# Kernel tuning notes

Hardware: AMD Instinct MI355X
Metric: run time of the kernel (lower is better)

Reference implementation:

```python
import jax, jax.numpy as jnp
import numpy as np

H = 512
V = 32000
B = 32
S = 64
T = 32  # max_len


def setup_inputs() -> dict:
    key = jax.random.key(0)
    ks = jax.random.split(key, 16)
    sc = 0.02
    return {
        'encoder_outputs': jax.random.normal(ks[0], (B, S, 2 * H), jnp.float32),
        'encoder_hidden': jax.random.normal(ks[1], (1, B, 2 * H), jnp.float32),
        'target_tensor': jax.random.randint(ks[2], (B, T), 0, V),
        'emb': sc * jax.random.normal(ks[3], (V, H), jnp.float32),
        'Wa_w': sc * jax.random.normal(ks[4], (H, H), jnp.float32),
        'Wa_b': jnp.zeros((H,), jnp.float32),
        'Ua_w': sc * jax.random.normal(ks[5], (H, 2 * H), jnp.float32),
        'Ua_b': jnp.zeros((H,), jnp.float32),
        'Va_w': sc * jax.random.normal(ks[6], (1, H), jnp.float32),
        'Va_b': jnp.zeros((1,), jnp.float32),
        'W_ih': sc * jax.random.normal(ks[7], (3 * H, 3 * H), jnp.float32),
        'b_ih': jnp.zeros((3 * H,), jnp.float32),
        'W_hh': sc * jax.random.normal(ks[8], (3 * H, H), jnp.float32),
        'b_hh': jnp.zeros((3 * H,), jnp.float32),
        'Wh': sc * jax.random.normal(ks[9], (H, 2 * H), jnp.float32),
        'bh': jnp.zeros((H,), jnp.float32),
        'out_w': sc * jax.random.normal(ks[10], (V, H), jnp.float32),
        'out_b': jnp.zeros((V,), jnp.float32),
    }


def reference(encoder_outputs, encoder_hidden, target_tensor, emb,
              Wa_w, Wa_b, Ua_w, Ua_b, Va_w, Va_b,
              W_ih, b_ih, W_hh, b_hh, Wh, bh, out_w, out_b):
    # initial hidden: Linear(2H -> H) applied to encoder_hidden [1,B,2H]
    h0 = encoder_hidden[0] @ Wh.T + bh  # [B,H]
    # Ua(keys) is step-invariant: precompute  [B,S,H]
    ua_keys = jnp.einsum('bsk,hk->bsh', encoder_outputs, Ua_w) + Ua_b
    # teacher forcing: first token is 0 (SOS), then shifted targets
    tokens = jnp.concatenate(
        [jnp.zeros((target_tensor.shape[0], 1), target_tensor.dtype),
         target_tensor[:, :-1]], axis=1)  # [B,T]

    def step(h, tok):
        x_emb = emb[tok]  # [B,H] (dropout is identity in eval)
        q = h @ Wa_w.T + Wa_b  # [B,H]
        e = jnp.tanh(q[:, None, :] + ua_keys)  # [B,S,H]
        scores = jnp.einsum('bsh,h->bs', e, Va_w[0]) + Va_b[0]  # [B,S]
        w = jax.nn.softmax(scores, axis=-1)  # [B,S]
        ctx = jnp.einsum('bs,bsk->bk', w, encoder_outputs)  # [B,2H]
        x = jnp.concatenate([x_emb, ctx], axis=-1)  # [B,3H]
        gx = x @ W_ih.T + b_ih  # [B,3H]
        gh = h @ W_hh.T + b_hh  # [B,3H]
        r = jax.nn.sigmoid(gx[:, :H] + gh[:, :H])
        z = jax.nn.sigmoid(gx[:, H:2 * H] + gh[:, H:2 * H])
        n = jnp.tanh(gx[:, 2 * H:] + r * gh[:, 2 * H:])
        h_new = (1.0 - z) * n + z * h
        logits = h_new @ out_w.T + out_b  # [B,V]
        return h_new, (logits, w)

    h_final, (logits, attn) = jax.lax.scan(step, h0, tokens.T)
    logits = jnp.transpose(logits, (1, 0, 2))  # [B,T,V]
    attn = jnp.transpose(attn, (1, 0, 2))  # [B,T,S]
    log_probs = jax.nn.log_softmax(logits, axis=-1)
    return log_probs, h_final[None], attn
```

## Files before the change

### kernel.cpp

```cpp
#include <hip/hip_runtime.h>
#include <hip/hip_bf16.h>

#define B_ 32
#define S_ 64
#define H_ 512
#define T_ 32
#define V_ 32000

typedef __attribute__((ext_vector_type(8))) short bf16x8;
typedef __attribute__((ext_vector_type(4))) float f32x4;

static __device__ __forceinline__ unsigned short f2bf(float f) {
    unsigned int u = __float_as_uint(f);
    u += 0x7FFF + ((u >> 16) & 1);
    return (unsigned short)(u >> 16);
}
static __device__ __forceinline__ float dot4(float4 a, float4 b) {
    return a.x * b.x + a.y * b.y + a.z * b.z + a.w * b.w;
}
static __device__ __forceinline__ float tanh_fast(float x) {
    x = fminf(fmaxf(x, -15.f), 15.f);
    float e = __expf(2.f * x);
    return (e - 1.f) / (e + 1.f);
}
static __device__ __forceinline__ float sigmoid_fast(float x) {
    return 1.f / (1.f + __expf(-x));
}

static __device__ __forceinline__ void gemm_tile_f32(
    const float* __restrict__ A, int Ald,
    const float* __restrict__ Bm, int Bld,
    const float* __restrict__ bias,
    float* __restrict__ C, int Cld,
    int m0, int n0, int k0beg, int k0end)
{
    __shared__ unsigned short As[128 * 32];
    __shared__ unsigned short Bs[128 * 32];

    const int tid  = threadIdx.x;
    const int lane = tid & 63;
    const int wave = tid >> 6;
    const int wm   = (wave & 1) * 64;
    const int wn   = (wave >> 1) * 64;
    const int quad = lane >> 4;
    const int l16  = lane & 15;

    f32x4 acc[4][4];
#pragma unroll
    for (int i = 0; i < 4; i++)
#pragma unroll
        for (int j = 0; j < 4; j++) acc[i][j] = (f32x4){0.f, 0.f, 0.f, 0.f};

    const int r0 = tid >> 2;
    const int q4 = tid & 3;

    for (int k0 = k0beg; k0 < k0end; k0 += 32) {
        __syncthreads();
#pragma unroll
        for (int rr = 0; rr < 2; rr++) {
            const int row = r0 + rr * 64;
            const float4 s0 = *(const float4*)(A + (size_t)(m0 + row) * Ald + k0 + q4 * 8);
            const float4 s1 = *(const float4*)(A + (size_t)(m0 + row) * Ald + k0 + q4 * 8 + 4);
            unsigned short tmp[8] = {f2bf(s0.x), f2bf(s0.y), f2bf(s0.z), f2bf(s0.w),
                                     f2bf(s1.x), f2bf(s1.y), f2bf(s1.z), f2bf(s1.w)};
            *(uint4*)(&As[row * 32 + q4 * 8]) = *(uint4*)tmp;
            const float4 t0 = *(const float4*)(Bm + (size_t)(n0 + row) * Bld + k0 + q4 * 8);
            const float4 t1 = *(const float4*)(Bm + (size_t)(n0 + row) * Bld + k0 + q4 * 8 + 4);
            unsigned short tb[8] = {f2bf(t0.x), f2bf(t0.y), f2bf(t0.z), f2bf(t0.w),
                                    f2bf(t1.x), f2bf(t1.y), f2bf(t1.z), f2bf(t1.w)};
            *(uint4*)(&Bs[row * 32 + q4 * 8]) = *(uint4*)tb;
        }
        __syncthreads();

        bf16x8 af[4], bfr[4];
#pragma unroll
        for (int i = 0; i < 4; i++)
            af[i] = *(const bf16x8*)(&As[(wm + 16 * i + l16) * 32 + quad * 8]);
#pragma unroll
        for (int j = 0; j < 4; j++)
            bfr[j] = *(const bf16x8*)(&Bs[(wn + 16 * j + l16) * 32 + quad * 8]);
#pragma unroll
        for (int i = 0; i < 4; i++)
#pragma unroll
            for (int j = 0; j < 4; j++)
                acc[i][j] = __builtin_amdgcn_mfma_f32_16x16x32_bf16(af[i], bfr[j], acc[i][j], 0, 0, 0);
    }

#pragma unroll
    for (int i = 0; i < 4; i++)
#pragma unroll
        for (int j = 0; j < 4; j++)
#pragma unroll
            for (int r = 0; r < 4; r++) {
                const int m = m0 + wm + 16 * i + quad * 4 + r;
                const int n = n0 + wn + 16 * j + l16;
                C[(size_t)m * Cld + n] = acc[i][j][r] + (bias ? bias[n] : 0.f);
            }
}

__global__ __launch_bounds__(256, 2)
void gemm_setup(const float* __restrict__ enc, const float* __restrict__ Xemb,
                const float* __restrict__ Ua_w, const float* __restrict__ W_ih,
                const float* __restrict__ b_ih,
                float* __restrict__ Pua, float* __restrict__ Gxe,
                float* __restrict__ Penc2)
{
    const int bid = blockIdx.x;
    if (bid < 128) {
        const int kk = bid & 1, l = bid >> 1;
        const int mt = l & 15, nt = l >> 4;
        gemm_tile_f32(enc, 1024, Ua_w, 1024, nullptr,
                      Pua + (size_t)kk * 1048576, 512,
                      mt * 128, nt * 128, kk * 512, kk * 512 + 512);
    } else if (bid < 224) {
        const int l = bid - 128;
        const int mt = l & 7, nt = l >> 3;
        gemm_tile_f32(Xemb, 512, W_ih, 1536, b_ih,
                      Gxe, 1536, mt * 128, nt * 128, 0, 512);
    } else {
        int l = bid - 224;
        const int kk = l & 1; l >>= 1;
        const int mt = l & 15, nt = l >> 4;
        gemm_tile_f32(enc, 1024, W_ih + 512, 1536, nullptr,
                      Penc2 + (size_t)kk * 3145728, 1536,
                      mt * 128, nt * 128, kk * 512, kk * 512 + 512);
    }
}

__global__ void k_combine(const float* __restrict__ Pua, const float* __restrict__ Ua_b,
                          float* __restrict__ ua, const float* __restrict__ Penc2,
                          float* __restrict__ ENC2)
{
    const int o = blockIdx.x * 256 + threadIdx.x;
    if (o < 262144) {
        const float4 a = ((const float4*)Pua)[o];
        const float4 b = ((const float4*)Pua)[262144 + o];
        const float4 bi = *(const float4*)(Ua_b + (o & 127) * 4);
        float4 r; r.x = a.x + b.x + bi.x; r.y = a.y + b.y + bi.y;
        r.z = a.z + b.z + bi.z; r.w = a.w + b.w + bi.w;
        ((float4*)ua)[o] = r;
    } else {
        const int i = o - 262144;
        const float4 a = ((const float4*)Penc2)[i];
        const float4 b = ((const float4*)Penc2)[786432 + i];
        float4 r; r.x = a.x + b.x; r.y = a.y + b.y; r.z = a.z + b.z; r.w = a.w + b.w;
        ((float4*)ENC2)[i] = r;
    }
}

__global__ __launch_bounds__(256, 2)
void gemm_logits(const unsigned short* __restrict__ A16, const float* __restrict__ Bm,
                 const float* __restrict__ bias, float* __restrict__ C)
{
    const int bid = blockIdx.x;
    const int xcd = bid & 7;
    const int l   = bid >> 3;
    const int nt  = (l >> 3) * 8 + xcd;
    if (nt >= 250) return;
    const int m0 = (l & 7) * 128;
    const int n0 = nt * 128;
    const int N = V_, K = 512, Bld = 512;

    __shared__ unsigned short As[128 * 32];
    __shared__ unsigned short Bs[128 * 32];

    const int tid  = threadIdx.x;
    const int lane = tid & 63;
    const int wave = tid >> 6;
    const int wm   = (wave & 1) * 64;
    const int wn   = (wave >> 1) * 64;
    const int quad = lane >> 4;
    const int l16  = lane & 15;

    f32x4 acc[4][4];
#pragma unroll
    for (int i = 0; i < 4; i++)
#pragma unroll
        for (int j = 0; j < 4; j++) acc[i][j] = (f32x4){0.f, 0.f, 0.f, 0.f};

    const int r0 = tid >> 2;
    const int q4 = tid & 3;

    for (int k0 = 0; k0 < K; k0 += 32) {
        __syncthreads();
#pragma unroll
        for (int rr = 0; rr < 2; rr++) {
            const int row = r0 + rr * 64;
            const uint4 v = *(const uint4*)(A16 + (size_t)(m0 + row) * K + k0 + q4 * 8);
            *(uint4*)(&As[row * 32 + q4 * 8]) = v;
            const float4 t0 = *(const float4*)(Bm + (size_t)(n0 + row) * Bld + k0 + q4 * 8);
            const float4 t1 = *(const float4*)(Bm + (size_t)(n0 + row) * Bld + k0 + q4 * 8 + 4);
            unsigned short tb[8] = {f2bf(t0.x), f2bf(t0.y), f2bf(t0.z), f2bf(t0.w),
                                    f2bf(t1.x), f2bf(t1.y), f2bf(t1.z), f2bf(t1.w)};
            *(uint4*)(&Bs[row * 32 + q4 * 8]) = *(uint4*)tb;
        }
        __syncthreads();

        bf16x8 af[4], bfr[4];
#pragma unroll
        for (int i = 0; i < 4; i++)
            af[i] = *(const bf16x8*)(&As[(wm + 16 * i + l16) * 32 + quad * 8]);
#pragma unroll
        for (int j = 0; j < 4; j++)
            bfr[j] = *(const bf16x8*)(&Bs[(wn + 16 * j + l16) * 32 + quad * 8]);
#pragma unroll
        for (int i = 0; i < 4; i++)
#pragma unroll
            for (int j = 0; j < 4; j++)
                acc[i][j] = __builtin_amdgcn_mfma_f32_16x16x32_bf16(af[i], bfr[j], acc[i][j], 0, 0, 0);
    }

#pragma unroll
    for (int i = 0; i < 4; i++)
#pragma unroll
        for (int j = 0; j < 4; j++)
#pragma unroll
            for (int r = 0; r < 4; r++) {
                const int m = m0 + wm + 16 * i + quad * 4 + r;
                const int n = n0 + wn + 16 * j + l16;
                C[(size_t)m * N + n] = acc[i][j][r] + bias[n];
            }
}

__global__ void k_h0part(const float* __restrict__ ehid, const float* __restrict__ Wh,
                         float* __restrict__ h0p)
{
    const int o = blockIdx.x * 256 + threadIdx.x;
    const int b = o & 31, j = (o >> 5) & 511, c = o >> 14;
    const float* x = ehid + b * 1024 + c * 256;
    const float* w = Wh + (size_t)j * 1024 + c * 256;
    float s = 0.f;
#pragma unroll 8
    for (int k = 0; k < 256; k += 4)
        s += dot4(*(const float4*)(x + k), *(const float4*)(w + k));
    h0p[c * 16384 + b * 512 + j] = s;
}

__global__ void k_h0fin(const float* __restrict__ h0p, const float* __restrict__ bh,
                        float* __restrict__ h)
{
    const int o = blockIdx.x * 256 + threadIdx.x;
    h[o] = bh[o & 511] + h0p[o] + h0p[16384 + o] + h0p[32768 + o] + h0p[49152 + o];
}

__global__ void k_gather(const float* __restrict__ emb, const int* __restrict__ tgt,
                         float* __restrict__ Xemb)
{
    const int o = blockIdx.x * 256 + threadIdx.x;
    const int r = o >> 7, k4 = (o & 127) * 4;
    const int b = r >> 5, t = r & 31;
    const int tok = t ? tgt[b * T_ + t - 1] : 0;
    *(float4*)(Xemb + (size_t)r * 512 + k4) = *(const float4*)(emb + (size_t)tok * 512 + k4);
}

__global__ __launch_bounds__(256)
void k_q_gh(const float* __restrict__ h, const float* __restrict__ Wa_w,
            const float* __restrict__ W_hh,
            float* __restrict__ qp, float* __restrict__ ghp)
{
    const int bid = blockIdx.x;
    const int tid = threadIdx.x;
    if (bid < 256) {
        const int o = bid * 256 + tid;
        const int b = o & 31, j = (o >> 5) & 511, c = o >> 14;
        const float* x = h + b * 512 + c * 128;
        const float* w = Wa_w + (size_t)j * 512 + c * 128;
        float s = 0.f;
#pragma unroll 8
        for (int k = 0; k < 128; k += 4)
            s += dot4(*(const float4*)(x + k), *(const float4*)(w + k));
        qp[c * 16384 + b * 512 + j] = s;
    } else {
        const int o = (bid - 256) * 256 + tid;
        const int b = o & 31, j = (o >> 5) & 511, c = o >> 14;
        const float* x  = h + b * 512 + c * 128;
        const float* w0 = W_hh + (size_t)j * 512 + c * 128;
        const float* w1 = w0 + 512 * 512;
        const float* w2 = w1 + 512 * 512;
        float s0 = 0.f, s1 = 0.f, s2 = 0.f;
#pragma unroll 8
        for (int k = 0; k < 128; k += 4) {
            const float4 xv = *(const float4*)(x + k);
            s0 += dot4(xv, *(const float4*)(w0 + k));
            s1 += dot4(xv, *(const float4*)(w1 + k));
            s2 += dot4(xv, *(const float4*)(w2 + k));
        }
        const int ix = b * 512 + j;
        ghp[(c * 3 + 0) * 16384 + ix] = s0;
        ghp[(c * 3 + 1) * 16384 + ix] = s1;
        ghp[(c * 3 + 2) * 16384 + ix] = s2;
    }
}

__global__ __launch_bounds__(256)
void k_attn_fin(const float* __restrict__ qp, const float* __restrict__ Wa_b,
                const float* __restrict__ ua, const float* __restrict__ Va_w,
                const float* __restrict__ Va_b, const float* __restrict__ ENC2,
                const float* __restrict__ ghp, const float* __restrict__ Gxe,
                const float* __restrict__ b_hh, float* __restrict__ h,
                unsigned short* __restrict__ Hall, float* __restrict__ attn_out,
                float* __restrict__ hf, int t)
{
    __shared__ float qs[512];
    __shared__ float parts[64][4];
    __shared__ float wsm[64];
    __shared__ float gxs[1536];

    const int b = blockIdx.x;
    const int tid = threadIdx.x;

    for (int i = tid; i < 512; i += 256) {
        const int ix = b * 512 + i;
        qs[i] = qp[ix] + qp[16384 + ix] + qp[32768 + ix] + qp[49152 + ix] + Wa_b[i];
    }
    __syncthreads();

    {
        const int s = tid >> 2, p = tid & 3;
        const float* uar = ua + ((size_t)(b * 64 + s)) * 512 + p * 128;
        const float* vp = Va_w + p * 128;
        float acc = 0.f;
#pragma unroll 8
        for (int k = 0; k < 128; k += 4) {
            float4 u4 = *(const float4*)(uar + k);
            float4 v4 = *(const float4*)(vp + k);
            float4 q4 = *(const float4*)(&qs[p * 128 + k]);
            acc += v4.x * tanh_fast(q4.x + u4.x) + v4.y * tanh_fast(q4.y + u4.y)
                 + v4.z * tanh_fast(q4.z + u4.z) + v4.w * tanh_fast(q4.w + u4.w);
        }
        parts[s][p] = acc;
    }
    __syncthreads();

    if (tid < 64) {
        float sc = parts[tid][0] + parts[tid][1] + parts[tid][2] + parts[tid][3] + Va_b[0];
        float mx = sc;
        for (int off = 32; off; off >>= 1) mx = fmaxf(mx, __shfl_down(mx, off));
        mx = __shfl(mx, 0);
        float e = __expf(sc - mx);
        float sum = e;
        for (int off = 32; off; off >>= 1) sum += __shfl_down(sum, off);
        sum = __shfl(sum, 0);
        float w = e / sum;
        wsm[tid] = w;
        attn_out[((size_t)b * T_ + t) * 64 + tid] = w;
    }
    __syncthreads();

    for (int i4 = tid; i4 < 384; i4 += 256) {
        float4 a = {0.f, 0.f, 0.f, 0.f};
        const float* eb = ENC2 + ((size_t)b * 64) * 1536 + i4 * 4;
        for (int s2 = 0; s2 < 64; s2++) {
            const float w = wsm[s2];
            const float4 e4 = *(const float4*)(eb + (size_t)s2 * 1536);
            a.x += w * e4.x; a.y += w * e4.y; a.z += w * e4.z; a.w += w * e4.w;
        }
        *(float4*)(&gxs[i4 * 4]) = a;
    }
    __syncthreads();

    for (int j = tid; j < 512; j += 256) {
        const int o2 = b * 512 + j;
        float gh0 = b_hh[j], gh1 = b_hh[512 + j], gh2 = b_hh[1024 + j];
#pragma unroll
        for (int c2 = 0; c2 < 4; c2++) {
            gh0 += ghp[(c2 * 3 + 0) * 16384 + o2];
            gh1 += ghp[(c2 * 3 + 1) * 16384 + o2];
            gh2 += ghp[(c2 * 3 + 2) * 16384 + o2];
        }
        const float* gxe = Gxe + ((size_t)(b * T_ + t)) * 1536;
        const float gx0 = gxs[j] + gxe[j];
        const float gx1 = gxs[512 + j] + gxe[512 + j];
        const float gx2 = gxs[1024 + j] + gxe[1024 + j];
        const float r = sigmoid_fast(gx0 + gh0);
        const float z = sigmoid_fast(gx1 + gh1);
        const float n = tanh_fast(gx2 + r * gh2);
        const float hn = (1.f - z) * n + z * h[o2];
        h[o2] = hn;
        Hall[((size_t)b * T_ + t) * 512 + j] = f2bf(hn);
        if (t == T_ - 1) hf[o2] = hn;
    }
}

__global__ void k_logsoftmax(float* __restrict__ logits)
{
    __shared__ float rm[4], rs[4];
    const int row = blockIdx.x;
    float* p = logits + (size_t)row * V_;
    const int tid = threadIdx.x;

    float m = -1e30f, s = 0.f;
    for (int i = tid * 4; i < V_; i += 1024) {
        const float4 x = *(const float4*)(p + i);
        const float m4 = fmaxf(fmaxf(x.x, x.y), fmaxf(x.z, x.w));
        const float mn = fmaxf(m, m4);
        s = s * __expf(m - mn) + __expf(x.x - mn) + __expf(x.y - mn)
          + __expf(x.z - mn) + __expf(x.w - mn);
        m = mn;
    }
    for (int off = 32; off; off >>= 1) {
        const float m2 = __shfl_down(m, off), s2 = __shfl_down(s, off);
        const float mn = fmaxf(m, m2);
        s = s * __expf(m - mn) + s2 * __expf(m2 - mn);
        m = mn;
    }
    if ((tid & 63) == 0) { rm[tid >> 6] = m; rs[tid >> 6] = s; }
    __syncthreads();
    const float M = fmaxf(fmaxf(rm[0], rm[1]), fmaxf(rm[2], rm[3]));
    const float S = rs[0] * __expf(rm[0] - M) + rs[1] * __expf(rm[1] - M)
                  + rs[2] * __expf(rm[2] - M) + rs[3] * __expf(rm[3] - M);
    const float lse = M + __logf(S);

    for (int i = tid * 4; i < V_; i += 1024) {
        float4 x = *(const float4*)(p + i);
        x.x -= lse; x.y -= lse; x.z -= lse; x.w -= lse;
        *(float4*)(p + i) = x;
    }
}

extern "C" void kernel_launch(void* const* d_in, const int* in_sizes, int n_in,
                              void* d_out, int out_size, void* d_ws, size_t ws_size,
                              hipStream_t stream)
{
    const float* enc   = (const float*)d_in[0];
    const float* ehid  = (const float*)d_in[1];
    const int*   tgt   = (const int*)d_in[2];
    const float* emb   = (const float*)d_in[3];
    const float* Wa_w  = (const float*)d_in[4];
    const float* Wa_b  = (const float*)d_in[5];
    const float* Ua_w  = (const float*)d_in[6];
    const float* Ua_b  = (const float*)d_in[7];
    const float* Va_w  = (const float*)d_in[8];
    const float* Va_b  = (const float*)d_in[9];
    const float* W_ih  = (const float*)d_in[10];
    const float* b_ih  = (const float*)d_in[11];
    const float* W_hh  = (const float*)d_in[12];
    const float* b_hh  = (const float*)d_in[13];
    const float* Wh    = (const float*)d_in[14];
    const float* bh    = (const float*)d_in[15];
    const float* out_w = (const float*)d_in[16];
    const float* out_b = (const float*)d_in[17];

    float* outp = (float*)d_out;
    float* lp   = outp;
    float* hf   = outp + 32768000;
    float* attn = outp + 32784384;

    float* Gxe   = lp;
    float* Xemb  = lp + 1572864;
    float* ghp   = lp + 2097152;
    float* qp    = lp + 2293760;
    float* ENC2  = lp + 2359296;
    float* h0p   = lp + 5505024;
    float* Pua   = lp + 5570560;
    float* Penc2 = lp + 7667712;

    float* ws  = (float*)d_ws;
    float* h   = ws;
    float* ua  = ws + 49152;
    unsigned short* Hall = (unsigned short*)(ws + 1097728);

    k_h0part<<<256, 256, 0, stream>>>(ehid, Wh, h0p);
    k_h0fin<<<64, 256, 0, stream>>>(h0p, bh, h);
    k_gather<<<512, 256, 0, stream>>>(emb, tgt, Xemb);
    gemm_setup<<<608, 256, 0, stream>>>(enc, Xemb, Ua_w, W_ih, b_ih,
                                        Pua, Gxe, Penc2);
    k_combine<<<4096, 256, 0, stream>>>(Pua, Ua_b, ua, Penc2, ENC2);

    for (int t = 0; t < T_; t++) {
        k_q_gh<<<512, 256, 0, stream>>>(h, Wa_w, W_hh, qp, ghp);
        k_attn_fin<<<32, 256, 0, stream>>>(qp, Wa_b, ua, Va_w, Va_b, ENC2,
                                           ghp, Gxe, b_hh, h, Hall, attn,
                                           hf, t);
    }

    gemm_logits<<<2048, 256, 0, stream>>>(Hall, out_w, out_b, lp);
    k_logsoftmax<<<1024, 256, 0, stream>>>(lp);
}
```

Before: 1.627 ms.

## Fuse setup kernels and split per-step attention across four blocks per batch

The embedding gather is folded into the Gxe GEMM tile loader, and the h0 projection and its reduction are merged into the setup GEMM and combine launches, removing three setup kernels. The per-step attention/GRU kernel now uses four blocks per batch row, each computing a quarter of the context and hidden outputs. The intent is fewer launches and more parallelism on the serial recurrence. The cost is that each of the four blocks recomputes the full attention scores and softmax.

```diff
diff --git a/kernel.cpp b/kernel.cpp
--- a/kernel.cpp
+++ b/kernel.cpp
@@ -98,12 +98,94 @@
             }
 }
 
+static __device__ __forceinline__ void gemm_tile_emb(
+    const float* __restrict__ emb, const int* __restrict__ tgt,
+    const float* __restrict__ Bm, int Bld,
+    const float* __restrict__ bias,
+    float* __restrict__ C, int Cld,
+    int m0, int n0)
+{
+    __shared__ unsigned short As[128 * 32];
+    __shared__ unsigned short Bs[128 * 32];
+
+    const int tid  = threadIdx.x;
+    const int lane = tid & 63;
+    const int wave = tid >> 6;
+    const int wm   = (wave & 1) * 64;
+    const int wn   = (wave >> 1) * 64;
+    const int quad = lane >> 4;
+    const int l16  = lane & 15;
+
+    f32x4 acc[4][4];
+#pragma unroll
+    for (int i = 0; i < 4; i++)
+#pragma unroll
+        for (int j = 0; j < 4; j++) acc[i][j] = (f32x4){0.f, 0.f, 0.f, 0.f};
+
+    const int r0 = tid >> 2;
+    const int q4 = tid & 3;
+
+    int tok[2];
+#pragma unroll
+    for (int rr = 0; rr < 2; rr++) {
+        const int r1 = m0 + r0 + rr * 64;
+        const int tt = r1 & 31, bb = r1 >> 5;
+        tok[rr] = tt ? tgt[bb * T_ + tt - 1] : 0;
+    }
+
+    for (int k0 = 0; k0 < 512; k0 += 32) {
+        __syncthreads();
+#pragma unroll
+        for (int rr = 0; rr < 2; rr++) {
+            const int row = r0 + rr * 64;
+            const float* arow = emb + (size_t)tok[rr] * 512;
+            const float4 s0 = *(const float4*)(arow + k0 + q4 * 8);
+            const float4 s1 = *(const float4*)(arow + k0 + q4 * 8 + 4);
+            unsigned short tmp[8] = {f2bf(s0.x), f2bf(s0.y), f2bf(s0.z), f2bf(s0.w),
+                                     f2bf(s1.x), f2bf(s1.y), f2bf(s1.z), f2bf(s1.w)};
+            *(uint4*)(&As[row * 32 + q4 * 8]) = *(uint4*)tmp;
+            const float4 t0 = *(const float4*)(Bm + (size_t)(n0 + row) * Bld + k0 + q4 * 8);
+            const float4 t1 = *(const float4*)(Bm + (size_t)(n0 + row) * Bld + k0 + q4 * 8 + 4);
+            unsigned short tb[8] = {f2bf(t0.x), f2bf(t0.y), f2bf(t0.z), f2bf(t0.w),
+                                    f2bf(t1.x), f2bf(t1.y), f2bf(t1.z), f2bf(t1.w)};
+            *(uint4*)(&Bs[row * 32 + q4 * 8]) = *(uint4*)tb;
+        }
+        __syncthreads();
+
+        bf16x8 af[4], bfr[4];
+#pragma unroll
+        for (int i = 0; i < 4; i++)
+            af[i] = *(const bf16x8*)(&As[(wm + 16 * i + l16) * 32 + quad * 8]);
+#pragma unroll
+        for (int j = 0; j < 4; j++)
+            bfr[j] = *(const bf16x8*)(&Bs[(wn + 16 * j + l16) * 32 + quad * 8]);
+#pragma unroll
+        for (int i = 0; i < 4; i++)
+#pragma unroll
+            for (int j = 0; j < 4; j++)
+                acc[i][j] = __builtin_amdgcn_mfma_f32_16x16x32_bf16(af[i], bfr[j], acc[i][j], 0, 0, 0);
+    }
+
+#pragma unroll
+    for (int i = 0; i < 4; i++)
+#pragma unroll
+        for (int j = 0; j < 4; j++)
+#pragma unroll
+            for (int r = 0; r < 4; r++) {
+                const int m = m0 + wm + 16 * i + quad * 4 + r;
+                const int n = n0 + wn + 16 * j + l16;
+                C[(size_t)m * Cld + n] = acc[i][j][r] + (bias ? bias[n] : 0.f);
+            }
+}
+
 __global__ __launch_bounds__(256, 2)
-void gemm_setup(const float* __restrict__ enc, const float* __restrict__ Xemb,
+void gemm_setup(const float* __restrict__ enc, const float* __restrict__ emb,
+                const int* __restrict__ tgt,
                 const float* __restrict__ Ua_w, const float* __restrict__ W_ih,
-                const float* __restrict__ b_ih,
+                const float* __restrict__ b_ih, const float* __restrict__ ehid,
+                const float* __restrict__ Wh,
                 float* __restrict__ Pua, float* __restrict__ Gxe,
-                float* __restrict__ Penc2)
+                float* __restrict__ Penc2, float* __restrict__ h0p)
 {
     const int bid = blockIdx.x;
     if (bid < 128) {
@@ -115,36 +197,53 @@
     } else if (bid < 224) {
         const int l = bid - 128;
         const int mt = l & 7, nt = l >> 3;
-        gemm_tile_f32(Xemb, 512, W_ih, 1536, b_ih,
-                      Gxe, 1536, mt * 128, nt * 128, 0, 512);
-    } else {
+        gemm_tile_emb(emb, tgt, W_ih, 1536, b_ih,
+                      Gxe, 1536, mt * 128, nt * 128);
+    } else if (bid < 608) {
         int l = bid - 224;
         const int kk = l & 1; l >>= 1;
         const int mt = l & 15, nt = l >> 4;
         gemm_tile_f32(enc, 1024, W_ih + 512, 1536, nullptr,
                       Penc2 + (size_t)kk * 3145728, 1536,
                       mt * 128, nt * 128, kk * 512, kk * 512 + 512);
+    } else {
+        const int o = (bid - 608) * 256 + threadIdx.x;
+        const int b = o & 31, j = (o >> 5) & 511, c = o >> 14;
+        const float* x = ehid + b * 1024 + c * 256;
+        const float* w = Wh + (size_t)j * 1024 + c * 256;
+        float s = 0.f;
+#pragma unroll 8
+        for (int k = 0; k < 256; k += 4)
+            s += dot4(*(const float4*)(x + k), *(const float4*)(w + k));
+        h0p[c * 16384 + b * 512 + j] = s;
     }
 }
 
 __global__ void k_combine(const float* __restrict__ Pua, const float* __restrict__ Ua_b,
                           float* __restrict__ ua, const float* __restrict__ Penc2,
-                          float* __restrict__ ENC2)
-{
-    const int o = blockIdx.x * 256 + threadIdx.x;
-    if (o < 262144) {
-        const float4 a = ((const float4*)Pua)[o];
-        const float4 b = ((const float4*)Pua)[262144 + o];
-        const float4 bi = *(const float4*)(Ua_b + (o & 127) * 4);
-        float4 r; r.x = a.x + b.x + bi.x; r.y = a.y + b.y + bi.y;
-        r.z = a.z + b.z + bi.z; r.w = a.w + b.w + bi.w;
-        ((float4*)ua)[o] = r;
+                          float* __restrict__ ENC2, const float* __restrict__ h0p,
+                          const float* __restrict__ bh, float* __restrict__ h)
+{
+    const int bid = blockIdx.x;
+    if (bid < 4096) {
+        const int o = bid * 256 + threadIdx.x;
+        if (o < 262144) {
+            const float4 a = ((const float4*)Pua)[o];
+            const float4 b = ((const float4*)Pua)[262144 + o];
+            const float4 bi = *(const float4*)(Ua_b + (o & 127) * 4);
+            float4 r; r.x = a.x + b.x + bi.x; r.y = a.y + b.y + bi.y;
+            r.z = a.z + b.z + bi.z; r.w = a.w + b.w + bi.w;
+            ((float4*)ua)[o] = r;
+        } else {
+            const int i = o - 262144;
+            const float4 a = ((const float4*)Penc2)[i];
+            const float4 b = ((const float4*)Penc2)[786432 + i];
+            float4 r; r.x = a.x + b.x; r.y = a.y + b.y; r.z = a.z + b.z; r.w = a.w + b.w;
+            ((float4*)ENC2)[i] = r;
+        }
     } else {
-        const int i = o - 262144;
-        const float4 a = ((const float4*)Penc2)[i];
-        const float4 b = ((const float4*)Penc2)[786432 + i];
-        float4 r; r.x = a.x + b.x; r.y = a.y + b.y; r.z = a.z + b.z; r.w = a.w + b.w;
-        ((float4*)ENC2)[i] = r;
+        const int o = (bid - 4096) * 256 + threadIdx.x;
+        h[o] = bh[o & 511] + h0p[o] + h0p[16384 + o] + h0p[32768 + o] + h0p[49152 + o];
     }
 }
 
@@ -220,37 +319,6 @@
                 const int n = n0 + wn + 16 * j + l16;
                 C[(size_t)m * N + n] = acc[i][j][r] + bias[n];
             }
-}
-
-__global__ void k_h0part(const float* __restrict__ ehid, const float* __restrict__ Wh,
-                         float* __restrict__ h0p)
-{
-    const int o = blockIdx.x * 256 + threadIdx.x;
-    const int b = o & 31, j = (o >> 5) & 511, c = o >> 14;
-    const float* x = ehid + b * 1024 + c * 256;
-    const float* w = Wh + (size_t)j * 1024 + c * 256;
-    float s = 0.f;
-#pragma unroll 8
-    for (int k = 0; k < 256; k += 4)
-        s += dot4(*(const float4*)(x + k), *(const float4*)(w + k));
-    h0p[c * 16384 + b * 512 + j] = s;
-}
-
-__global__ void k_h0fin(const float* __restrict__ h0p, const float* __restrict__ bh,
-                        float* __restrict__ h)
-{
-    const int o = blockIdx.x * 256 + threadIdx.x;
-    h[o] = bh[o & 511] + h0p[o] + h0p[16384 + o] + h0p[32768 + o] + h0p[49152 + o];
-}
-
-__global__ void k_gather(const float* __restrict__ emb, const int* __restrict__ tgt,
-                         float* __restrict__ Xemb)
-{
-    const int o = blockIdx.x * 256 + threadIdx.x;
-    const int r = o >> 7, k4 = (o & 127) * 4;
-    const int b = r >> 5, t = r & 31;
-    const int tok = t ? tgt[b * T_ + t - 1] : 0;
-    *(float4*)(Xemb + (size_t)r * 512 + k4) = *(const float4*)(emb + (size_t)tok * 512 + k4);
 }
 
 __global__ __launch_bounds__(256)
@@ -306,7 +374,8 @@
     __shared__ float wsm[64];
     __shared__ float gxs[1536];
 
-    const int b = blockIdx.x;
+    const int bid = blockIdx.x;
+    const int b = bid >> 2, part = bid & 3;
     const int tid = threadIdx.x;
 
     for (int i = tid; i < 512; i += 256) {
@@ -343,11 +412,13 @@
         sum = __shfl(sum, 0);
         float w = e / sum;
         wsm[tid] = w;
-        attn_out[((size_t)b * T_ + t) * 64 + tid] = w;
+        if (part == 0) attn_out[((size_t)b * T_ + t) * 64 + tid] = w;
     }
     __syncthreads();
 
-    for (int i4 = tid; i4 < 384; i4 += 256) {
+    if (tid < 96) {
+        const int g = tid >> 5, u = tid & 31;
+        const int i4 = g * 128 + part * 32 + u;
         float4 a = {0.f, 0.f, 0.f, 0.f};
         const float* eb = ENC2 + ((size_t)b * 64) * 1536 + i4 * 4;
         for (int s2 = 0; s2 < 64; s2++) {
@@ -359,7 +430,8 @@
     }
     __syncthreads();
 
-    for (int j = tid; j < 512; j += 256) {
+    if (tid < 128) {
+        const int j = part * 128 + tid;
         const int o2 = b * 512 + j;
         float gh0 = b_hh[j], gh1 = b_hh[512 + j], gh2 = b_hh[1024 + j];
 #pragma unroll
@@ -447,7 +519,6 @@
     float* attn = outp + 32784384;
 
     float* Gxe   = lp;
-    float* Xemb  = lp + 1572864;
     float* ghp   = lp + 2097152;
     float* qp    = lp + 2293760;
     float* ENC2  = lp + 2359296;
@@ -460,18 +531,16 @@
     float* ua  = ws + 49152;
     unsigned short* Hall = (unsigned short*)(ws + 1097728);
 
-    k_h0part<<<256, 256, 0, stream>>>(ehid, Wh, h0p);
-    k_h0fin<<<64, 256, 0, stream>>>(h0p, bh, h);
-    k_gather<<<512, 256, 0, stream>>>(emb, tgt, Xemb);
-    gemm_setup<<<608, 256, 0, stream>>>(enc, Xemb, Ua_w, W_ih, b_ih,
-                                        Pua, Gxe, Penc2);
-    k_combine<<<4096, 256, 0, stream>>>(Pua, Ua_b, ua, Penc2, ENC2);
+    gemm_setup<<<864, 256, 0, stream>>>(enc, emb, tgt, Ua_w, W_ih, b_ih,
+                                        ehid, Wh, Pua, Gxe, Penc2, h0p);
+    k_combine<<<4160, 256, 0, stream>>>(Pua, Ua_b, ua, Penc2, ENC2,
+                                        h0p, bh, h);
 
     for (int t = 0; t < T_; t++) {
         k_q_gh<<<512, 256, 0, stream>>>(h, Wa_w, W_hh, qp, ghp);
-        k_attn_fin<<<32, 256, 0, stream>>>(qp, Wa_b, ua, Va_w, Va_b, ENC2,
-                                           ghp, Gxe, b_hh, h, Hall, attn,
-                                           hf, t);
+        k_attn_fin<<<128, 256, 0, stream>>>(qp, Wa_b, ua, Va_w, Va_b, ENC2,
+                                            ghp, Gxe, b_hh, h, Hall, attn,
+                                            hf, t);
     }
 
     gemm_logits<<<2048, 256, 0, stream>>>(Hall, out_w, out_b, lp);
```

After: 1.391 ms. 1.17x faster.
